# Optimization experiments

Measured on AMD Instinct MI355X. Metric: run time of the kernel, lower is better.

Reference implementation:

```python
import jax, jax.numpy as jnp
import numpy as np

VOCAB = 30
D_MODEL = 512
D_K = 64
D_V = 64
N_HEAD = 8
D_FF = 2048
N_LAYERS = 4
LN_EPS = 1e-5


def _make_pe(max_len, d_model):
    pos = np.arange(max_len, dtype=np.float32)[:, None]
    div = np.exp(np.arange(0, d_model, 2, dtype=np.float32) * (-np.log(10000.0) / d_model))
    pe = np.zeros((max_len, d_model), dtype=np.float32)
    pe[:, 0::2] = np.sin(pos * div)
    pe[:, 1::2] = np.cos(pos * div)
    return jnp.asarray(pe)


def setup_inputs() -> dict:
    key = jax.random.key(0)
    ks = jax.random.split(key, 16)
    B, S = 4, 2048
    s = 0.02
    inp = {
        "input_ids": jax.random.randint(ks[0], (B, S), 0, VOCAB, dtype=jnp.int64),
        "attn_mask": jax.random.randint(ks[1], (B, S), 0, 2, dtype=jnp.int64),
        "tok_embed": jax.random.normal(ks[2], (VOCAB, D_MODEL), jnp.float32) * s,
        "pe": _make_pe(S, D_MODEL),
        "Wq": jax.random.normal(ks[3], (N_LAYERS, D_MODEL, N_HEAD * D_K), jnp.float32) * s,
        "Wk": jax.random.normal(ks[4], (N_LAYERS, D_MODEL, N_HEAD * D_K), jnp.float32) * s,
        "Wv": jax.random.normal(ks[5], (N_LAYERS, D_MODEL, N_HEAD * D_V), jnp.float32) * s,
        "Wo": jax.random.normal(ks[6], (N_LAYERS, N_HEAD * D_V, D_MODEL), jnp.float32) * s,
        "ln1_g": jnp.ones((N_LAYERS, D_MODEL), jnp.float32),
        "ln1_b": jnp.zeros((N_LAYERS, D_MODEL), jnp.float32),
        "W1": jax.random.normal(ks[7], (N_LAYERS, D_MODEL, D_FF), jnp.float32) * s,
        "W2": jax.random.normal(ks[8], (N_LAYERS, D_FF, D_MODEL), jnp.float32) * s,
        "ln2_g": jnp.ones((N_LAYERS, D_MODEL), jnp.float32),
        "ln2_b": jnp.zeros((N_LAYERS, D_MODEL), jnp.float32),
    }
    return inp


def _layernorm(x, g, b):
    mu = jnp.mean(x, axis=-1, keepdims=True)
    var = jnp.mean(jnp.square(x - mu), axis=-1, keepdims=True)
    return (x - mu) * jax.lax.rsqrt(var + LN_EPS) * g + b


def reference(input_ids, attn_mask, tok_embed, pe, Wq, Wk, Wv, Wo, ln1_g, ln1_b, W1, W2, ln2_g, ln2_b):
    B, S = input_ids.shape
    x = tok_embed[input_ids] + pe[:S][None]  # [B,S,D]
    # pad mask: key positions where attn_mask==0, broadcast over heads & queries
    pad = (attn_mask == 0)[:, None, None, :]  # [B,1,1,S]
    scale = 1.0 / np.sqrt(D_K)
    for l in range(N_LAYERS):
        # multi-head self-attention
        q = (x @ Wq[l]).reshape(B, S, N_HEAD, D_K)
        k = (x @ Wk[l]).reshape(B, S, N_HEAD, D_K)
        v = (x @ Wv[l]).reshape(B, S, N_HEAD, D_V)
        scores = jnp.einsum('bqhd,bkhd->bhqk', q, k) * scale
        scores = jnp.where(pad, -1e9, scores)
        attn = jax.nn.softmax(scores, axis=-1)
        ctx = jnp.einsum('bhqk,bkhd->bqhd', attn, v).reshape(B, S, N_HEAD * D_V)
        x = _layernorm(ctx @ Wo[l] + x, ln1_g[l], ln1_b[l])
        # position-wise FFN
        h = jax.nn.relu(x @ W1[l])
        x = _layernorm(h @ W2[l] + x, ln2_g[l], ln2_b[l])
    return x
```

## Files before the change

kernel.cpp:

```cpp
#include <hip/hip_runtime.h>
#include <stdint.h>

#define S_LEN 2048
#define B_SZ 4
#define DM 512
#define NTOK (B_SZ * S_LEN)

typedef unsigned short u16;
typedef unsigned int u32;
typedef unsigned long long u64;
typedef __attribute__((ext_vector_type(8))) short short8;
typedef __attribute__((ext_vector_type(4))) float f32x4;

typedef const __attribute__((address_space(1))) u32 gq_t;
typedef __attribute__((address_space(3))) u32 lq_t;

__device__ __forceinline__ u16 f2bf(float f) {
  union { float f; u32 u; } v; v.f = f;
  return (u16)((v.u + 0x7FFFu + ((v.u >> 16) & 1u)) >> 16);
}

__device__ __forceinline__ float bf2f(u32 hi16_at_lo) {
  union { u32 u; float f; } v; v.u = hi16_at_lo;
  return v.f;
}

__device__ __forceinline__ float fexp2(float x) {
#if __has_builtin(__builtin_amdgcn_exp2f)
  return __builtin_amdgcn_exp2f(x);
#else
  return exp2f(x);
#endif
}

__device__ __forceinline__ short8 mk8(u64 a, u64 b) {
  union { u64 q[2]; short8 s; } u;
  u.q[0] = a; u.q[1] = b;
  return u.s;
}

__device__ __forceinline__ void swap32(u32& x, u32& y) {
  asm("v_permlane32_swap_b32 %0, %1" : "+v"(x), "+v"(y));
}
__device__ __forceinline__ void swap16(u32& x, u32& y, int lane) {
#if __has_builtin(__builtin_amdgcn_permlane16_swap)
  asm("v_permlane16_swap_b32 %0, %1" : "+v"(x), "+v"(y));
#else
  u32 tx = __builtin_amdgcn_ds_swizzle(x, 0x401F);
  u32 ty = __builtin_amdgcn_ds_swizzle(y, 0x401F);
  bool up = (lane & 16) != 0;
  u32 nx = up ? ty : x;
  u32 ny = up ? y : tx;
  x = nx; y = ny;
#endif
}

__global__ void embed_kernel(const int* __restrict__ ids, const float* __restrict__ te,
                             const float* __restrict__ pe, u16* __restrict__ xb) {
  int gid = blockIdx.x * 256 + threadIdx.x;
  int tok = gid >> 7, c4 = (gid & 127) << 2;
  int s = tok & (S_LEN - 1);
  int id = ids[tok];
  const float4 a = *(const float4*)(te + (long)id * DM + c4);
  const float4 p = *(const float4*)(pe + (long)s * DM + c4);
  uint2 pk;
  pk.x = (u32)f2bf(a.x + p.x) | ((u32)f2bf(a.y + p.y) << 16);
  pk.y = (u32)f2bf(a.z + p.z) | ((u32)f2bf(a.w + p.w) << 16);
  *(uint2*)(xb + (long)tok * DM + c4) = pk;
}

__global__ void wconv_all(const float* __restrict__ Wq, const float* __restrict__ Wk,
                          const float* __restrict__ Wv, const float* __restrict__ Wo,
                          const float* __restrict__ W1, const float* __restrict__ W2,
                          u16* __restrict__ WqkvT, u16* __restrict__ WoT,
                          u16* __restrict__ W1T, u16* __restrict__ W2T) {
  __shared__ u16 t_lds[64 * 65];
  const int tile = blockIdx.x;
  const float* src; u16* dst; int N, K, kt, nt, l;
  if (tile < 768) {
    int which = tile >> 8, r = tile & 255;
    l = r >> 6; int rr = r & 63; kt = rr >> 3; nt = rr & 7;
    src = (which == 0 ? Wq : which == 1 ? Wk : Wv) + (long)l * 512 * 512;
    N = 512; K = 512;
    dst = WqkvT + (long)l * 1536 * 512 + (long)(which * 512) * 512;
  } else if (tile < 1024) {
    int r = tile - 768;
    l = r >> 6; int rr = r & 63; kt = rr >> 3; nt = rr & 7;
    src = Wo + (long)l * 512 * 512; N = 512; K = 512;
    dst = WoT + (long)l * 512 * 512;
  } else if (tile < 2048) {
    int r = tile - 1024;
    l = r >> 8; int rr = r & 255; kt = rr >> 5; nt = rr & 31;
    src = W1 + (long)l * 512 * 2048; N = 2048; K = 512;
    dst = W1T + (long)l * 2048 * 512;
  } else {
    int r = tile - 2048;
    l = r >> 8; int rr = r & 255; kt = rr >> 3; nt = rr & 7;
    src = W2 + (long)l * 2048 * 512; N = 512; K = 2048;
    dst = W2T + (long)l * 512 * 2048;
  }
  const int tr = threadIdx.x >> 4;
  const int tc = (threadIdx.x & 15) << 2;
#pragma unroll
  for (int i = 0; i < 4; ++i) {
    int k = tr + i * 16;
    const float4 v = *(const float4*)(src + (long)(kt * 64 + k) * N + nt * 64 + tc);
    t_lds[(tc + 0) * 65 + k] = f2bf(v.x);
    t_lds[(tc + 1) * 65 + k] = f2bf(v.y);
    t_lds[(tc + 2) * 65 + k] = f2bf(v.z);
    t_lds[(tc + 3) * 65 + k] = f2bf(v.w);
  }
  __syncthreads();
#pragma unroll
  for (int i = 0; i < 4; ++i) {
    int n = tr + i * 16;
    u16 a0 = t_lds[n * 65 + tc + 0];
    u16 a1 = t_lds[n * 65 + tc + 1];
    u16 a2 = t_lds[n * 65 + tc + 2];
    u16 a3 = t_lds[n * 65 + tc + 3];
    uint2 pk;
    pk.x = (u32)a0 | ((u32)a1 << 16);
    pk.y = (u32)a2 | ((u32)a3 << 16);
    *(uint2*)(dst + (long)(nt * 64 + n) * K + kt * 64 + tc) = pk;
  }
}

template <int BM, int BN, bool RELU, bool VSPLIT, bool SWAPC>
__global__ __launch_bounds__(BM * 2) void gemm_kernel(const u16* __restrict__ A,
                                                      const u16* __restrict__ BT,
                                                      void* __restrict__ Cout,
                                                      u16* __restrict__ vt,
                                                      int M, int N, int K) {
  constexpr int NI = BN / 32;
  constexpr int NW = BM / 32;
  constexpr int BRW = BN / NW;
  constexpr int LOADS = 4 + BRW / 8;
  __shared__ __align__(16) u16 a_t[2][BM * 64];
  __shared__ __align__(16) u16 b_t[2][BN * 64];
  const int tid = threadIdx.x;
  const int w = tid >> 6, lane = tid & 63;
  const int wr = w >> 1, wc = w & 1;
  const int g = lane >> 4, lr = lane & 15;
  const int l8 = lane >> 3, lch = lane & 7;
  const int gc = lch ^ l8;
  const int nwg = gridDim.x * gridDim.y;
  const int bid = blockIdx.x + gridDim.x * blockIdx.y;
  const int cpx = nwg >> 3;
  const int swz = (bid & 7) * cpx + (bid >> 3);
  const int bx = swz % gridDim.x, by = swz / gridDim.x;
  const long m0 = (long)by * BM, n0 = (long)bx * BN;
  f32x4 acc[4][NI] = {};
  const int nk = K >> 6;

  auto stage = [&](int nb, int kt) {
    const int k0 = kt << 6;
#pragma unroll
    for (int i = 0; i < 4; ++i) {
      int row = w * 32 + i * 8 + l8;
      __builtin_amdgcn_global_load_lds((gq_t*)(A + (m0 + row) * K + k0 + gc * 8),
                                       (lq_t*)&a_t[nb][(w * 4 + i) * 512], 16, 0, 0);
    }
#pragma unroll
    for (int i = 0; i < BRW / 8; ++i) {
      int row = w * BRW + i * 8 + l8;
      __builtin_amdgcn_global_load_lds((gq_t*)(BT + (n0 + row) * K + k0 + gc * 8),
                                       (lq_t*)&b_t[nb][(w * (BRW / 8) + i) * 512], 16, 0, 0);
    }
  };

  stage(0, 0);
  stage(1, 1);
  for (int kt = 0; kt < nk; ++kt) {
    const int cur = kt & 1;
    if (kt + 1 < nk) {
      if constexpr (LOADS == 6) asm volatile("s_waitcnt vmcnt(6)" ::: "memory");
      else                      asm volatile("s_waitcnt vmcnt(5)" ::: "memory");
    } else {
      asm volatile("s_waitcnt vmcnt(0)" ::: "memory");
    }
    __builtin_amdgcn_s_barrier();
    __builtin_amdgcn_sched_barrier(0);
    short8 af[2][4], bfr[2][NI];
#pragma unroll
    for (int ks = 0; ks < 2; ++ks) {
#pragma unroll
      for (int mi = 0; mi < 4; ++mi) {
        int row = wr * 64 + mi * 16 + lr;
        int byte = row * 128 + (((ks * 4 + g) ^ (row & 7)) << 4);
        af[ks][mi] = *(const short8*)((const char*)a_t[cur] + byte);
      }
#pragma unroll
      for (int ni = 0; ni < NI; ++ni) {
        int row = wc * (BN / 2) + ni * 16 + lr;
        int byte = row * 128 + (((ks * 4 + g) ^ (row & 7)) << 4);
        bfr[ks][ni] = *(const short8*)((const char*)b_t[cur] + byte);
      }
    }
    asm volatile("s_waitcnt lgkmcnt(0)" ::: "memory");
    __builtin_amdgcn_s_barrier();
    __builtin_amdgcn_sched_barrier(0);
    if (kt + 2 < nk) stage(cur, kt + 2);
#pragma unroll
    for (int ks = 0; ks < 2; ++ks)
#pragma unroll
      for (int mi = 0; mi < 4; ++mi)
#pragma unroll
        for (int ni = 0; ni < NI; ++ni) {
          if constexpr (SWAPC)
            acc[mi][ni] = __builtin_amdgcn_mfma_f32_16x16x32_bf16(bfr[ks][ni], af[ks][mi], acc[mi][ni], 0, 0, 0);
          else
            acc[mi][ni] = __builtin_amdgcn_mfma_f32_16x16x32_bf16(af[ks][mi], bfr[ks][ni], acc[mi][ni], 0, 0, 0);
        }
  }

  if constexpr (VSPLIT) {
    if (n0 >= 1024) {
#pragma unroll
      for (int mi = 0; mi < 4; ++mi)
#pragma unroll
        for (int ni = 0; ni < NI; ++ni) {
          int vc = (int)(n0 - 1024) + wc * (BN / 2) + ni * 16 + lr;
          int hh = vc >> 6, d = vc & 63;
          long tok0 = m0 + wr * 64 + mi * 16 + g * 4;
          int bb = (int)(tok0 >> 11), s0 = (int)(tok0 & 2047);
          uint2 pk;
          pk.x = (u32)f2bf(acc[mi][ni][0]) | ((u32)f2bf(acc[mi][ni][1]) << 16);
          pk.y = (u32)f2bf(acc[mi][ni][2]) | ((u32)f2bf(acc[mi][ni][3]) << 16);
          *(uint2*)(vt + (((long)bb * 8 + hh) * 64 + d) * 2048 + s0) = pk;
        }
      return;
    }
  }
  if constexpr (SWAPC) {
#pragma unroll
    for (int mi = 0; mi < 4; ++mi)
#pragma unroll
      for (int ni = 0; ni < NI; ++ni) {
        long grow = m0 + wr * 64 + mi * 16 + lr;
        long gcb = n0 + wc * (BN / 2) + ni * 16 + 4 * g;
        float v0 = acc[mi][ni][0], v1 = acc[mi][ni][1], v2 = acc[mi][ni][2], v3 = acc[mi][ni][3];
        if (RELU) {
          v0 = fmaxf(v0, 0.f); v1 = fmaxf(v1, 0.f); v2 = fmaxf(v2, 0.f); v3 = fmaxf(v3, 0.f);
        }
        uint2 pk;
        pk.x = (u32)f2bf(v0) | ((u32)f2bf(v1) << 16);
        pk.y = (u32)f2bf(v2) | ((u32)f2bf(v3) << 16);
        *(uint2*)((u16*)Cout + grow * N + gcb) = pk;
      }
  } else {
#pragma unroll
    for (int mi = 0; mi < 4; ++mi)
#pragma unroll
      for (int ni = 0; ni < NI; ++ni)
#pragma unroll
        for (int j = 0; j < 4; ++j) {
          long grow = m0 + wr * 64 + mi * 16 + g * 4 + j;
          long gcol = n0 + wc * (BN / 2) + ni * 16 + lr;
          float v = acc[mi][ni][j];
          if (RELU) v = fmaxf(v, 0.f);
          ((u16*)Cout)[grow * N + gcol] = f2bf(v);
        }
  }
}

__global__ __launch_bounds__(512) void attn_kernel(const u16* __restrict__ qkv,
                                                   const u16* __restrict__ vt,
                                                   const int* __restrict__ mask,
                                                   u16* __restrict__ ctx) {
  __shared__ __align__(16) u16 k_t[2][64 * 64];
  __shared__ __align__(16) u16 v_t[2][80 * 64];
  __shared__ __align__(16) u16 q_t[128 * 64];
  __shared__ __align__(16) float mvals[2][64];
  __shared__ __align__(16) float l_lds[128];
  const int tid = threadIdx.x;
  const int w = tid >> 6, lane = tid & 63;
  const int g = lane >> 4, lr = lane & 15;
  const int l8 = lane >> 3, lch = lane & 7;
  const int gc = lch ^ l8;
  const int b = blockIdx.z, h = blockIdx.y, q0 = blockIdx.x * 128;
  const long base = (long)b * S_LEN * 1536;
  const int qcol = h * 64, kcol = 512 + h * 64;
  const u16* vhead = vt + (((long)b * 8 + h) * 64) * 2048;
  const float SC = 0.18033688011112042f;

  auto stageKV = [&](int nb, int kb) {
    {
      int row = w * 8 + l8;
      __builtin_amdgcn_global_load_lds((gq_t*)(qkv + base + (long)(kb + row) * 1536 + kcol + gc * 8),
                                       (lq_t*)&k_t[nb][w * 512], 16, 0, 0);
    }
    {
      int row = w * 8 + l8;
      __builtin_amdgcn_global_load_lds((gq_t*)(vhead + (long)row * 2048 + kb + gc * 8),
                                       (lq_t*)&v_t[nb][w * 512], 16, 0, 0);
    }
    if (tid < 64) mvals[nb][tid] = (mask[b * S_LEN + kb + tid] == 0) ? -1e9f : 0.f;
  };

  {
    int r16 = tid >> 5;
    u32 val = (r16 == 0) ? 0x3F803F80u : 0u;
    *(u32*)((char*)v_t[0] + 64 * 128 + tid * 4) = val;
    *(u32*)((char*)v_t[1] + 64 * 128 + tid * 4) = val;
  }
#pragma unroll
  for (int i = 0; i < 2; ++i) {
    int e = i * 512 + tid;
    int row = e >> 3, ch = e & 7;
    uint4 v = *(const uint4*)(qkv + base + (long)(q0 + row) * 1536 + qcol + ch * 8);
    *(uint4*)((char*)q_t + row * 128 + ((ch ^ (row & 7)) << 4)) = v;
  }
  stageKV(0, 0);
  __syncthreads();
  short8 qf[2];
#pragma unroll
  for (int ks = 0; ks < 2; ++ks) {
    int row = w * 16 + lr;
    qf[ks] = *(const short8*)((const char*)q_t + row * 128 + (((ks * 4 + g) ^ (row & 7)) << 4));
  }

  f32x4 o[5] = {};

  for (int kt = 0; kt < S_LEN / 64; ++kt) {
    const int cur = kt & 1;
    if (kt + 1 < S_LEN / 64) stageKV(cur ^ 1, (kt + 1) * 64);

    f32x4 s[4] = {};
#pragma unroll
    for (int ks = 0; ks < 2; ++ks) {
#pragma unroll
      for (int ni = 0; ni < 4; ++ni) {
        int row = ni * 16 + lr;
        short8 kf = *(const short8*)((const char*)k_t[cur] + row * 128 + (((ks * 4 + g) ^ (row & 7)) << 4));
        s[ni] = __builtin_amdgcn_mfma_f32_16x16x32_bf16(kf, qf[ks], s[ni], 0, 0, 0);
      }
    }
    float p[4][4];
#pragma unroll
    for (int ni = 0; ni < 4; ++ni) {
      const float4 mv = *(const float4*)&mvals[cur][ni * 16 + 4 * g];
      const float mva[4] = {mv.x, mv.y, mv.z, mv.w};
#pragma unroll
      for (int r = 0; r < 4; ++r)
        p[ni][r] = fexp2(fmaf(s[ni][r], SC, mva[r]));
    }
    u32 wv[4][2];
#pragma unroll
    for (int ni = 0; ni < 4; ++ni)
#pragma unroll
      for (int pp = 0; pp < 2; ++pp)
        asm("v_cvt_pk_bf16_f32 %0, %1, %2"
            : "=v"(wv[ni][pp]) : "v"(p[ni][2 * pp]), "v"(p[ni][2 * pp + 1]));

    u32 x0 = wv[0][0], x1 = wv[0][1], y0 = wv[1][0], y1 = wv[1][1];
    swap32(x0, y0); swap32(x1, y1);
    swap16(x0, y0, lane); swap16(x1, y1, lane);
    short8 pa0 = mk8((u64)x0 | ((u64)x1 << 32), (u64)y0 | ((u64)y1 << 32));
    u32 x2 = wv[2][0], x3 = wv[2][1], y2 = wv[3][0], y3 = wv[3][1];
    swap32(x2, y2); swap32(x3, y3);
    swap16(x2, y2, lane); swap16(x3, y3, lane);
    short8 pa1 = mk8((u64)x2 | ((u64)x3 << 32), (u64)y2 | ((u64)y3 << 32));

#pragma unroll
    for (int ks2 = 0; ks2 < 2; ++ks2) {
      short8 pa = ks2 ? pa1 : pa0;
#pragma unroll
      for (int nd = 0; nd < 5; ++nd) {
        int vrow = nd * 16 + lr;
        short8 vf = *(const short8*)((const char*)v_t[cur] + vrow * 128 + (((ks2 * 4 + g) ^ (vrow & 7)) << 4));
        o[nd] = __builtin_amdgcn_mfma_f32_16x16x32_bf16(pa, vf, o[nd], 0, 0, 0);
      }
    }
    if (kt + 1 < S_LEN / 64) __syncthreads();
  }
  if (lr == 0) {
#pragma unroll
    for (int r = 0; r < 4; ++r) l_lds[w * 16 + 4 * g + r] = o[4][r];
  }
  const float4 lv = *(const float4*)&l_lds[w * 16 + 4 * g];
  const float la[4] = {lv.x, lv.y, lv.z, lv.w};
  float inv[4];
#pragma unroll
  for (int r = 0; r < 4; ++r) inv[r] = 1.f / la[r];
#pragma unroll
  for (int nd = 0; nd < 4; ++nd)
#pragma unroll
    for (int r = 0; r < 4; ++r) {
      int tok = q0 + w * 16 + 4 * g + r;
      int col = h * 64 + nd * 16 + lr;
      ctx[((long)b * S_LEN + tok) * 512 + col] = f2bf(o[nd][r] * inv[r]);
    }
}

template <bool FINAL>
__global__ __launch_bounds__(256) void ln_kernel(const u16* __restrict__ y,
                                                 const u16* __restrict__ res,
                                                 const float* __restrict__ gam,
                                                 const float* __restrict__ bet,
                                                 u16* __restrict__ xout,
                                                 float* __restrict__ outf) {
  const int row = blockIdx.x, t = threadIdx.x;
  const long o0 = (long)row * DM;
  const u32 yb = *(const u32*)(y + o0 + 2 * t);
  const u32 rb = *(const u32*)(res + o0 + 2 * t);
  float a0 = bf2f(yb << 16) + bf2f(rb << 16);
  float a1 = bf2f(yb & 0xFFFF0000u) + bf2f(rb & 0xFFFF0000u);
  float s1 = a0 + a1, s2 = a0 * a0 + a1 * a1;
#pragma unroll
  for (int m = 32; m >= 1; m >>= 1) {
    s1 += __shfl_xor(s1, m);
    s2 += __shfl_xor(s2, m);
  }
  __shared__ float w1[4], w2[4];
  if ((t & 63) == 0) { w1[t >> 6] = s1; w2[t >> 6] = s2; }
  __syncthreads();
  s1 = w1[0] + w1[1] + w1[2] + w1[3];
  s2 = w2[0] + w2[1] + w2[2] + w2[3];
  const float mu = s1 * (1.f / DM);
  const float rstd = rsqrtf(s2 * (1.f / DM) - mu * mu + 1e-5f);
  const float2 gv = *(const float2*)&gam[2 * t];
  const float2 bv = *(const float2*)&bet[2 * t];
  float r0 = (a0 - mu) * rstd * gv.x + bv.x;
  float r1 = (a1 - mu) * rstd * gv.y + bv.y;
  if constexpr (FINAL) {
    float2 ov; ov.x = r0; ov.y = r1;
    *(float2*)&outf[o0 + 2 * t] = ov;
  } else {
    u32 pk = (u32)f2bf(r0) | ((u32)f2bf(r1) << 16);
    *(u32*)&xout[o0 + 2 * t] = pk;
  }
}

extern "C" void kernel_launch(void* const* d_in, const int* in_sizes, int n_in,
                              void* d_out, int out_size, void* d_ws, size_t ws_size,
                              hipStream_t stream) {
  const int*   ids  = (const int*)d_in[0];
  const int*   amsk = (const int*)d_in[1];
  const float* te   = (const float*)d_in[2];
  const float* pe   = (const float*)d_in[3];
  const float* Wq   = (const float*)d_in[4];
  const float* Wk   = (const float*)d_in[5];
  const float* Wv   = (const float*)d_in[6];
  const float* Wo   = (const float*)d_in[7];
  const float* ln1g = (const float*)d_in[8];
  const float* ln1b = (const float*)d_in[9];
  const float* W1   = (const float*)d_in[10];
  const float* W2   = (const float*)d_in[11];
  const float* ln2g = (const float*)d_in[12];
  const float* ln2b = (const float*)d_in[13];
  float* out = (float*)d_out;

  char* p = (char*)d_ws;
  u16* x     = (u16*)p;   p += (long)NTOK * DM * 2;
  u16* qkv   = (u16*)p;   p += (long)NTOK * 1536 * 2;
  u16* ctx   = (u16*)p;   p += (long)NTOK * DM * 2;
  u16* tmp   = (u16*)p;   p += (long)NTOK * DM * 2;
  u16* hb    = (u16*)p;   p += (long)NTOK * 2048 * 2;
  u16* WqkvT = (u16*)p;   p += (long)4 * 1536 * 512 * 2;
  u16* WoT   = (u16*)p;   p += (long)4 * 512 * 512 * 2;
  u16* W1T   = (u16*)p;   p += (long)4 * 2048 * 512 * 2;
  u16* W2T   = (u16*)p;   p += (long)4 * 512 * 2048 * 2;
  if ((size_t)(p - (char*)d_ws) > ws_size) return;
  u16* vt = hb;

  wconv_all<<<3072, 256, 0, stream>>>(Wq, Wk, Wv, Wo, W1, W2, WqkvT, WoT, W1T, W2T);
  embed_kernel<<<NTOK * 128 / 256, 256, 0, stream>>>(ids, te, pe, x);

  for (int l = 0; l < 4; ++l) {
    gemm_kernel<256, 64, false, true, false><<<dim3(1536 / 64, NTOK / 256), 512, 0, stream>>>(
        x, WqkvT + (long)l * 1536 * 512, qkv, vt, NTOK, 1536, 512);
    attn_kernel<<<dim3(S_LEN / 128, 8, B_SZ), 512, 0, stream>>>(qkv, vt, amsk, ctx);
    gemm_kernel<128, 64, false, false, true><<<dim3(512 / 64, NTOK / 128), 256, 0, stream>>>(
        ctx, WoT + (long)l * 512 * 512, tmp, nullptr, NTOK, 512, 512);
    ln_kernel<false><<<NTOK, 256, 0, stream>>>(tmp, x, ln1g + l * 512, ln1b + l * 512, x, nullptr);
    gemm_kernel<256, 64, true, false, true><<<dim3(2048 / 64, NTOK / 256), 512, 0, stream>>>(
        x, W1T + (long)l * 2048 * 512, hb, nullptr, NTOK, 2048, 512);
    gemm_kernel<128, 64, false, false, true><<<dim3(512 / 64, NTOK / 128), 256, 0, stream>>>(
        hb, W2T + (long)l * 512 * 2048, tmp, nullptr, NTOK, 512, 2048);
    if (l == 3)
      ln_kernel<true><<<NTOK, 256, 0, stream>>>(tmp, x, ln2g + l * 512, ln2b + l * 512, nullptr, out);
    else
      ln_kernel<false><<<NTOK, 256, 0, stream>>>(tmp, x, ln2g + l * 512, ln2b + l * 512, x, nullptr);
  }
}
```

Baseline: 599.7 us.

## Split attention over two key halves and merge partial outputs

The attention kernel now processes only half of the key sequence per block, doubling the grid from 512 to 1024 blocks. Each half writes unnormalized bf16 partial outputs and row sums, and a new merge kernel adds them and normalizes. LDS is consolidated: Q staging shares space with the K/V buffers and the ones-row for the sum is stored once. This raises occupancy and parallelism (the same no-running-max exp scheme is kept) at the cost of an extra kernel launch, extra global traffic, and bf16 rounding of the unnormalized partials.

New measurement: 629.8 us. 1.05x slower.

```diff
diff --git a/kernel.cpp b/kernel.cpp
--- a/kernel.cpp
+++ b/kernel.cpp
@@ -266,42 +266,38 @@
 __global__ __launch_bounds__(512) void attn_kernel(const u16* __restrict__ qkv,
                                                    const u16* __restrict__ vt,
                                                    const int* __restrict__ mask,
-                                                   u16* __restrict__ ctx) {
-  __shared__ __align__(16) u16 k_t[2][64 * 64];
-  __shared__ __align__(16) u16 v_t[2][80 * 64];
-  __shared__ __align__(16) u16 q_t[128 * 64];
+                                                   u16* __restrict__ o0dst,
+                                                   u16* __restrict__ o1dst,
+                                                   float* __restrict__ lbuf) {
+  __shared__ __align__(16) u16 kv[2 * 4096 + 2 * 4096 + 1024];
   __shared__ __align__(16) float mvals[2][64];
-  __shared__ __align__(16) float l_lds[128];
   const int tid = threadIdx.x;
   const int w = tid >> 6, lane = tid & 63;
   const int g = lane >> 4, lr = lane & 15;
   const int l8 = lane >> 3, lch = lane & 7;
   const int gc = lch ^ l8;
-  const int b = blockIdx.z, h = blockIdx.y, q0 = blockIdx.x * 128;
+  const int half = blockIdx.x & 1, q0 = (blockIdx.x >> 1) * 128;
+  const int b = blockIdx.z, h = blockIdx.y;
+  const int kb0 = half * 1024;
   const long base = (long)b * S_LEN * 1536;
   const int qcol = h * 64, kcol = 512 + h * 64;
   const u16* vhead = vt + (((long)b * 8 + h) * 64) * 2048;
+  u16* q_t = kv;
+  u16* vone = kv + 16384;
   const float SC = 0.18033688011112042f;
 
   auto stageKV = [&](int nb, int kb) {
-    {
-      int row = w * 8 + l8;
-      __builtin_amdgcn_global_load_lds((gq_t*)(qkv + base + (long)(kb + row) * 1536 + kcol + gc * 8),
-                                       (lq_t*)&k_t[nb][w * 512], 16, 0, 0);
-    }
-    {
-      int row = w * 8 + l8;
-      __builtin_amdgcn_global_load_lds((gq_t*)(vhead + (long)row * 2048 + kb + gc * 8),
-                                       (lq_t*)&v_t[nb][w * 512], 16, 0, 0);
-    }
+    int row = w * 8 + l8;
+    __builtin_amdgcn_global_load_lds((gq_t*)(qkv + base + (long)(kb + row) * 1536 + kcol + gc * 8),
+                                     (lq_t*)(kv + nb * 4096 + w * 512), 16, 0, 0);
+    __builtin_amdgcn_global_load_lds((gq_t*)(vhead + (long)row * 2048 + kb + gc * 8),
+                                     (lq_t*)(kv + 8192 + nb * 4096 + w * 512), 16, 0, 0);
     if (tid < 64) mvals[nb][tid] = (mask[b * S_LEN + kb + tid] == 0) ? -1e9f : 0.f;
   };
 
   {
-    int r16 = tid >> 5;
-    u32 val = (r16 == 0) ? 0x3F803F80u : 0u;
-    *(u32*)((char*)v_t[0] + 64 * 128 + tid * 4) = val;
-    *(u32*)((char*)v_t[1] + 64 * 128 + tid * 4) = val;
+    u32 val = ((tid >> 5) == 0) ? 0x3F803F80u : 0u;
+    *(u32*)((char*)vone + tid * 4) = val;
   }
 #pragma unroll
   for (int i = 0; i < 2; ++i) {
@@ -310,7 +306,6 @@
     uint4 v = *(const uint4*)(qkv + base + (long)(q0 + row) * 1536 + qcol + ch * 8);
     *(uint4*)((char*)q_t + row * 128 + ((ch ^ (row & 7)) << 4)) = v;
   }
-  stageKV(0, 0);
   __syncthreads();
   short8 qf[2];
 #pragma unroll
@@ -318,12 +313,15 @@
     int row = w * 16 + lr;
     qf[ks] = *(const short8*)((const char*)q_t + row * 128 + (((ks * 4 + g) ^ (row & 7)) << 4));
   }
+  __syncthreads();
+  stageKV(0, kb0);
+  __syncthreads();
 
   f32x4 o[5] = {};
 
-  for (int kt = 0; kt < S_LEN / 64; ++kt) {
+  for (int kt = 0; kt < 16; ++kt) {
     const int cur = kt & 1;
-    if (kt + 1 < S_LEN / 64) stageKV(cur ^ 1, (kt + 1) * 64);
+    if (kt + 1 < 16) stageKV(cur ^ 1, kb0 + (kt + 1) * 64);
 
     f32x4 s[4] = {};
 #pragma unroll
@@ -331,7 +329,7 @@
 #pragma unroll
       for (int ni = 0; ni < 4; ++ni) {
         int row = ni * 16 + lr;
-        short8 kf = *(const short8*)((const char*)k_t[cur] + row * 128 + (((ks * 4 + g) ^ (row & 7)) << 4));
+        short8 kf = *(const short8*)((const char*)(kv + cur * 4096) + row * 128 + (((ks * 4 + g) ^ (row & 7)) << 4));
         s[ni] = __builtin_amdgcn_mfma_f32_16x16x32_bf16(kf, qf[ks], s[ni], 0, 0, 0);
       }
     }
@@ -366,30 +364,55 @@
       short8 pa = ks2 ? pa1 : pa0;
 #pragma unroll
       for (int nd = 0; nd < 5; ++nd) {
-        int vrow = nd * 16 + lr;
-        short8 vf = *(const short8*)((const char*)v_t[cur] + vrow * 128 + (((ks2 * 4 + g) ^ (vrow & 7)) << 4));
+        short8 vf;
+        if (nd < 4) {
+          int vrow = nd * 16 + lr;
+          vf = *(const short8*)((const char*)(kv + 8192 + cur * 4096) + vrow * 128 + (((ks2 * 4 + g) ^ (vrow & 7)) << 4));
+        } else {
+          vf = *(const short8*)((const char*)vone + lr * 128 + (((ks2 * 4 + g) ^ (lr & 7)) << 4));
+        }
         o[nd] = __builtin_amdgcn_mfma_f32_16x16x32_bf16(pa, vf, o[nd], 0, 0, 0);
       }
     }
-    if (kt + 1 < S_LEN / 64) __syncthreads();
+    if (kt + 1 < 16) __syncthreads();
   }
   if (lr == 0) {
 #pragma unroll
-    for (int r = 0; r < 4; ++r) l_lds[w * 16 + 4 * g + r] = o[4][r];
-  }
-  const float4 lv = *(const float4*)&l_lds[w * 16 + 4 * g];
-  const float la[4] = {lv.x, lv.y, lv.z, lv.w};
-  float inv[4];
-#pragma unroll
-  for (int r = 0; r < 4; ++r) inv[r] = 1.f / la[r];
+    for (int r = 0; r < 4; ++r) {
+      int tok = q0 + w * 16 + 4 * g + r;
+      lbuf[(((long)(half * 4 + b)) * 2048 + tok) * 8 + h] = o[4][r];
+    }
+  }
+  u16* dst = half ? o1dst : o0dst;
 #pragma unroll
   for (int nd = 0; nd < 4; ++nd)
 #pragma unroll
     for (int r = 0; r < 4; ++r) {
       int tok = q0 + w * 16 + 4 * g + r;
       int col = h * 64 + nd * 16 + lr;
-      ctx[((long)b * S_LEN + tok) * 512 + col] = f2bf(o[nd][r] * inv[r]);
-    }
+      dst[((long)b * S_LEN + tok) * 512 + col] = f2bf(o[nd][r]);
+    }
+}
+
+__global__ void attn_merge(const u16* __restrict__ o0, const u16* __restrict__ o1,
+                           const float* __restrict__ lbuf, u16* __restrict__ dst) {
+  int gid = blockIdx.x * 256 + threadIdx.x;
+  int tok = gid >> 7, c4 = (gid & 127) << 2;
+  int h = c4 >> 6;
+  int b = tok >> 11, s = tok & 2047;
+  float l1 = lbuf[(((long)b) * 2048 + s) * 8 + h];
+  float l2 = lbuf[(((long)(4 + b)) * 2048 + s) * 8 + h];
+  float inv = 1.f / (l1 + l2);
+  uint2 a = *(const uint2*)(o0 + (long)tok * 512 + c4);
+  uint2 c = *(const uint2*)(o1 + (long)tok * 512 + c4);
+  float r0 = (bf2f(a.x << 16) + bf2f(c.x << 16)) * inv;
+  float r1 = (bf2f(a.x & 0xFFFF0000u) + bf2f(c.x & 0xFFFF0000u)) * inv;
+  float r2 = (bf2f(a.y << 16) + bf2f(c.y << 16)) * inv;
+  float r3 = (bf2f(a.y & 0xFFFF0000u) + bf2f(c.y & 0xFFFF0000u)) * inv;
+  uint2 pk;
+  pk.x = (u32)f2bf(r0) | ((u32)f2bf(r1) << 16);
+  pk.y = (u32)f2bf(r2) | ((u32)f2bf(r3) << 16);
+  *(uint2*)(dst + (long)tok * 512 + c4) = pk;
 }
 
 template <bool FINAL>
@@ -460,6 +483,7 @@
   u16* WoT   = (u16*)p;   p += (long)4 * 512 * 512 * 2;
   u16* W1T   = (u16*)p;   p += (long)4 * 2048 * 512 * 2;
   u16* W2T   = (u16*)p;   p += (long)4 * 512 * 2048 * 2;
+  float* lbuf = (float*)p; p += (long)2 * B_SZ * S_LEN * 8 * 4;
   if ((size_t)(p - (char*)d_ws) > ws_size) return;
   u16* vt = hb;
 
@@ -469,9 +493,10 @@
   for (int l = 0; l < 4; ++l) {
     gemm_kernel<256, 64, false, true, false><<<dim3(1536 / 64, NTOK / 256), 512, 0, stream>>>(
         x, WqkvT + (long)l * 1536 * 512, qkv, vt, NTOK, 1536, 512);
-    attn_kernel<<<dim3(S_LEN / 128, 8, B_SZ), 512, 0, stream>>>(qkv, vt, amsk, ctx);
+    attn_kernel<<<dim3(S_LEN / 128 * 2, 8, B_SZ), 512, 0, stream>>>(qkv, vt, amsk, ctx, tmp, lbuf);
+    attn_merge<<<NTOK * 128 / 256, 256, 0, stream>>>(ctx, tmp, lbuf, qkv);
     gemm_kernel<128, 64, false, false, true><<<dim3(512 / 64, NTOK / 128), 256, 0, stream>>>(
-        ctx, WoT + (long)l * 512 * 512, tmp, nullptr, NTOK, 512, 512);
+        qkv, WoT + (long)l * 512 * 512, tmp, nullptr, NTOK, 512, 512);
     ln_kernel<false><<<NTOK, 256, 0, stream>>>(tmp, x, ln1g + l * 512, ln1b + l * 512, x, nullptr);
     gemm_kernel<256, 64, true, false, true><<<dim3(2048 / 64, NTOK / 256), 512, 0, stream>>>(
         x, W1T + (long)l * 2048 * 512, hb, nullptr, NTOK, 2048, 512);
```
